# Performance work log

Hardware: AMD Instinct MI355X
Metric: run time of the kernel (lower is better)

The kernel has to match this reference:

```python
import jax, jax.numpy as jnp
import numpy as np

N = 262144   # number of samples (graph edges)
D = 32       # in_features; 'delta_t' is column 0
H = D - 1    # hidden width of each bucket MLP
K = 21       # number of time buckets


def setup_inputs() -> dict:
    key = jax.random.key(0)
    ks = jax.random.split(key, 7)
    x = jax.random.uniform(ks[0], (N, D), dtype=jnp.float32)
    x = x.at[:, 0].set(x[:, 0] * 2.1)  # delta_t in (0, 2.1] -> hits all 21 buckets
    s = 1.0 / np.sqrt(H).astype(np.float32)
    a = jax.random.normal(ks[1], (H,), jnp.float32)           # FeatureTransform scale a_i
    b = jax.random.normal(ks[2], (H,), jnp.float32) * 0.1     # FeatureTransform bias b_i
    W1 = jax.random.normal(ks[3], (K, H, H), jnp.float32) * s # layer_blocks weights
    b1 = jax.random.normal(ks[4], (K, H), jnp.float32) * s
    W2 = jax.random.normal(ks[5], (K, H), jnp.float32) * s    # layer_blocks2 weights (out=1)
    b2 = jax.random.normal(ks[6], (K,), jnp.float32) * s
    return {"x": x, "a": a, "b": b, "W1": W1, "b1": b1, "W2": W2, "b2": b2}


def reference(x, a, b, W1, b1, W2, b2):
    # delta_t column is NOT feature-transformed; all other columns are.
    # Note: the torch code mutates x in place, so x_without_t sees the
    # transformed features while t is the raw delta_t.
    t = x[:, 0]                                   # [N]
    feats = x[:, 1:] * a + b                      # FeatureTransform: a_i*x_i + b_i, [N,H]
    # All 21 bucket branches: Linear -> LeakyReLU(0.1) -> Linear(H,1)
    h = jnp.einsum('nd,kde->kne', feats, W1) + b1[:, None, :]   # [K,N,H]
    h = jnp.where(h >= 0, h, 0.1 * h)                           # LeakyReLU(0.1)
    out = jnp.einsum('kne,ke->kn', h, W2) + b2[:, None]         # [K,N]
    # bucket mask: start < t <= end with edges 0.0,0.1,...,2.0,1000
    edges = jnp.concatenate([jnp.arange(K, dtype=jnp.float32) / 10.0,
                             jnp.array([1000.0], dtype=jnp.float32)])
    valid = (t[None, :] > edges[:-1, None]) & (t[None, :] <= edges[1:, None])  # [K,N]
    return (out * valid.astype(out.dtype)).sum(axis=0)[:, None]  # [N,1]
```

## Files before the change

### kernel.cpp

```cpp
#include <hip/hip_runtime.h>
#include <hip/hip_bf16.h>

#define NN 262144
#define DD 32
#define HH 31
#define KK 21
#define ROWS 256
#define FSTRIDE 18

typedef __attribute__((ext_vector_type(8))) short bf16x8;
typedef __attribute__((ext_vector_type(4))) float f32x4;
typedef __attribute__((ext_vector_type(2))) unsigned int u32x2;
typedef __attribute__((ext_vector_type(4))) unsigned int u32x4;

static __device__ __forceinline__ unsigned short f2bf(float f) {
    __hip_bfloat16 h = __float2bfloat16(f);
    return __builtin_bit_cast(unsigned short, h);
}
static __device__ __forceinline__ unsigned pack2(float lo, float hi) {
    return (unsigned)f2bf(lo) | ((unsigned)f2bf(hi) << 16);
}

__global__ __launch_bounds__(64) void prep_kernel(
    const float* __restrict__ W1, const float* __restrict__ b1,
    const float* __restrict__ W2,
    bf16x8* __restrict__ A0tab, bf16x8* __restrict__ A1tab,
    f32x4* __restrict__ cq0b, f32x4* __restrict__ cq0w,
    f32x4* __restrict__ cq1b, f32x4* __restrict__ cq1w)
{
    const int k = (int)blockIdx.x;
    const int lane = (int)threadIdx.x;
    const int lrow = lane & 15, lgrp = lane >> 4;
    const float* __restrict__ W1k = W1 + k * HH * HH;
    const int e0 = lrow, e1 = 16 + lrow;

    bf16x8 A0, A1;
    #pragma unroll
    for (int j = 0; j < 4; ++j) {
        const int d1 = 4 * lgrp + j;
        const int d2 = 16 + 4 * lgrp + j;
        A0[j]     = (short)f2bf(W1k[d1 * HH + e0]);
        A0[4 + j] = (d2 < HH) ? (short)f2bf(W1k[d2 * HH + e0]) : (short)0;
        A1[j]     = (e1 < HH) ? (short)f2bf(W1k[d1 * HH + e1]) : (short)0;
        A1[4 + j] = (e1 < HH && d2 < HH) ? (short)f2bf(W1k[d2 * HH + e1]) : (short)0;
    }
    A0tab[k * 64 + lane] = A0;
    A1tab[k * 64 + lane] = A1;

    f32x4 b0v, w0v, b1v, w1v;
    #pragma unroll
    for (int r = 0; r < 4; ++r) {
        const int e = 4 * lgrp + r, eb = 16 + e;
        b0v[r] = b1[k * HH + e];
        w0v[r] = W2[k * HH + e];
        b1v[r] = (eb < HH) ? b1[k * HH + eb] : 0.0f;
        w1v[r] = (eb < HH) ? W2[k * HH + eb] : 0.0f;
    }
    cq0b[k * 64 + lane] = b0v;
    cq0w[k * 64 + lane] = w0v;
    cq1b[k * 64 + lane] = b1v;
    cq1w[k * 64 + lane] = w1v;
}

__global__ __launch_bounds__(256, 6) void fused_kernel(
    const float* __restrict__ x,
    const float* __restrict__ a,
    const float* __restrict__ b,
    const float* __restrict__ b2,
    const bf16x8* __restrict__ A0tab, const bf16x8* __restrict__ A1tab,
    const f32x4* __restrict__ cq0b, const f32x4* __restrict__ cq0w,
    const f32x4* __restrict__ cq1b, const f32x4* __restrict__ cq1w,
    float* __restrict__ out)
{
    __shared__ unsigned fbf[ROWS * FSTRIDE];
    __shared__ int cnt[KK];
    __shared__ int rnk[KK];
    __shared__ int sbase[KK];
    __shared__ int tstart[KK + 1];
    __shared__ unsigned short sorted[ROWS];

    const int tid = (int)threadIdx.x;
    const int rowbase = (int)blockIdx.x * ROWS;

    if (tid < KK) { cnt[tid] = 0; rnk[tid] = 0; }
    __syncthreads();

    const float* __restrict__ xr = x + (size_t)(rowbase + tid) * DD;
    float4 c[8];
    #pragma unroll
    for (int i = 0; i < 8; ++i) c[i] = ((const float4*)xr)[i];
    const float t = c[0].x;

    const float edges[KK + 1] = {
        0.0f, 0.1f, 0.2f, 0.3f, 0.4f, 0.5f, 0.6f, 0.7f, 0.8f, 0.9f, 1.0f,
        1.1f, 1.2f, 1.3f, 1.4f, 1.5f, 1.6f, 1.7f, 1.8f, 1.9f, 2.0f, 1000.0f
    };
    int kq = -1;
    #pragma unroll
    for (int j = 0; j < KK; ++j)
        if (t > edges[j] && t <= edges[j + 1]) kq = j;

    unsigned* __restrict__ frow = fbf + tid * FSTRIDE;
    #pragma unroll
    for (int s = 0; s < 8; ++s) {
        const float f0 = fmaf(c[s].y, a[4 * s + 0], b[4 * s + 0]);
        const float f1 = fmaf(c[s].z, a[4 * s + 1], b[4 * s + 1]);
        const float f2 = fmaf(c[s].w, a[4 * s + 2], b[4 * s + 2]);
        const float f3 = (s < 7) ? fmaf(c[s + 1].x, a[4 * s + 3], b[4 * s + 3]) : 0.0f;
        frow[2 * s]     = pack2(f0, f1);
        frow[2 * s + 1] = pack2(f2, f3);
    }

    if (kq >= 0) atomicAdd(&cnt[kq], 1);
    else out[rowbase + tid] = 0.0f;
    __syncthreads();

    if (tid == 0) {
        int s = 0, ts = 0;
        #pragma unroll
        for (int j = 0; j < KK; ++j) {
            sbase[j] = s; tstart[j] = ts;
            s += cnt[j]; ts += (cnt[j] + 15) >> 4;
        }
        tstart[KK] = ts;
    }
    __syncthreads();
    if (kq >= 0) {
        const int r = atomicAdd(&rnk[kq], 1);
        sorted[sbase[kq] + r] = (unsigned short)tid;
    }
    __syncthreads();

    const int lane = tid & 63;
    const int wave = tid >> 6;
    const int lrow = lane & 15;
    const int lgrp = lane >> 4;

    const int NT = tstart[KK];
    const int ts_l = tstart[(lane <= KK) ? lane : KK];

    for (int tix = wave; tix < NT; tix += 4) {
        const unsigned long long m = __ballot(ts_l <= tix);
        const int k = __builtin_amdgcn_readfirstlane(__popcll(m) - 1);

        const int sb = sbase[k];
        const int cn = cnt[k];
        const int r0 = (tix - tstart[k]) * 16;
        const int rl = r0 + lrow;

        const int R = sorted[sb + ((rl < cn) ? rl : 0)];

        const unsigned* __restrict__ fr = fbf + R * FSTRIDE;
        const u32x2 wlo = *(const u32x2*)(fr + 2 * lgrp);
        const u32x2 whi = *(const u32x2*)(fr + 8 + 2 * lgrp);
        u32x4 bw;
        bw[0] = wlo[0]; bw[1] = wlo[1]; bw[2] = whi[0]; bw[3] = whi[1];
        const bf16x8 B = __builtin_bit_cast(bf16x8, bw);

        const bf16x8 A0 = A0tab[k * 64 + lane];
        const bf16x8 A1 = A1tab[k * 64 + lane];
        const f32x4 cb0 = cq0b[k * 64 + lane];
        const f32x4 cw0 = cq0w[k * 64 + lane];
        const f32x4 cb1 = cq1b[k * 64 + lane];
        const f32x4 cw1 = cq1w[k * 64 + lane];
        const float b2k = b2[k];

        f32x4 acc0 = {0.0f, 0.0f, 0.0f, 0.0f};
        f32x4 acc1 = {0.0f, 0.0f, 0.0f, 0.0f};
        acc0 = __builtin_amdgcn_mfma_f32_16x16x32_bf16(A0, B, acc0, 0, 0, 0);
        acc1 = __builtin_amdgcn_mfma_f32_16x16x32_bf16(A1, B, acc1, 0, 0, 0);

        float S = 0.0f;
        #pragma unroll
        for (int r = 0; r < 4; ++r) {
            const float h0 = acc0[r] + cb0[r];
            const float q0 = (h0 >= 0.0f) ? h0 : 0.1f * h0;
            S = fmaf(q0, cw0[r], S);
            const float h1 = acc1[r] + cb1[r];
            const float q1 = (h1 >= 0.0f) ? h1 : 0.1f * h1;
            S = fmaf(q1, cw1[r], S);
        }
        S += __shfl_xor(S, 16);
        S += __shfl_xor(S, 32);

        if (lgrp == 0 && rl < cn) out[rowbase + R] = S + b2k;
    }
}

extern "C" void kernel_launch(void* const* d_in, const int* in_sizes, int n_in,
                              void* d_out, int out_size, void* d_ws, size_t ws_size,
                              hipStream_t stream) {
    const float* x  = (const float*)d_in[0];
    const float* a  = (const float*)d_in[1];
    const float* b  = (const float*)d_in[2];
    const float* W1 = (const float*)d_in[3];
    const float* b1 = (const float*)d_in[4];
    const float* W2 = (const float*)d_in[5];
    const float* b2 = (const float*)d_in[6];
    float* out = (float*)d_out;

    char* ws = (char*)d_ws;
    bf16x8* A0tab = (bf16x8*)ws;
    bf16x8* A1tab = A0tab + KK * 64;
    f32x4* cq0b = (f32x4*)(A1tab + KK * 64);
    f32x4* cq0w = cq0b + KK * 64;
    f32x4* cq1b = cq0w + KK * 64;
    f32x4* cq1w = cq1b + KK * 64;

    hipLaunchKernelGGL(prep_kernel, dim3(KK), dim3(64), 0, stream,
                       W1, b1, W2, A0tab, A1tab, cq0b, cq0w, cq1b, cq1w);

    hipLaunchKernelGGL(fused_kernel, dim3(NN / ROWS), dim3(256), 0, stream,
                       x, a, b, b2, A0tab, A1tab, cq0b, cq0w, cq1b, cq1w, out);
}
```

Baseline: 21.38 us.

## Split each row across two threads, halve rows per block, parallel-scan bucket offsets

Each block now handles 128 rows with 256 threads, so two threads share a row and each loads half of it (four float4s) and transforms sixteen features; the missing boundary element comes from a lane shuffle. The serial single-thread prefix over bucket counts becomes a wave-level shuffle scan, and the occupancy hint rises to 8 blocks per SM. The aim is fewer registers per thread, more latency hiding on the x loads, and a shorter serial section. The cost is twice as many blocks, each with fewer 16-row MFMA tiles, so partially filled bucket tiles make up a larger share of the work.

```diff
diff --git a/kernel.cpp b/kernel.cpp
--- a/kernel.cpp
+++ b/kernel.cpp
@@ -5,7 +5,7 @@
 #define DD 32
 #define HH 31
 #define KK 21
-#define ROWS 256
+#define ROWS 128
 #define FSTRIDE 18
 
 typedef __attribute__((ext_vector_type(8))) short bf16x8;
@@ -62,7 +62,7 @@
     cq1w[k * 64 + lane] = w1v;
 }
 
-__global__ __launch_bounds__(256, 6) void fused_kernel(
+__global__ __launch_bounds__(256, 8) void fused_kernel(
     const float* __restrict__ x,
     const float* __restrict__ a,
     const float* __restrict__ b,
@@ -80,17 +80,23 @@
     __shared__ unsigned short sorted[ROWS];
 
     const int tid = (int)threadIdx.x;
+    const int lane = tid & 63;
     const int rowbase = (int)blockIdx.x * ROWS;
 
     if (tid < KK) { cnt[tid] = 0; rnk[tid] = 0; }
     __syncthreads();
 
-    const float* __restrict__ xr = x + (size_t)(rowbase + tid) * DD;
-    float4 c[8];
-    #pragma unroll
-    for (int i = 0; i < 8; ++i) c[i] = ((const float4*)xr)[i];
+    const int r    = tid >> 1;
+    const int half = tid & 1;
+    const float4* __restrict__ p =
+        reinterpret_cast<const float4*>(x) + (size_t)blockIdx.x * (ROWS * DD / 4) + tid * 4;
+    float4 c[4];
+    #pragma unroll
+    for (int i = 0; i < 4; ++i) c[i] = p[i];
+
+    const float e16 = __shfl(c[0].x, lane + 1);
+
     const float t = c[0].x;
-
     const float edges[KK + 1] = {
         0.0f, 0.1f, 0.2f, 0.3f, 0.4f, 0.5f, 0.6f, 0.7f, 0.8f, 0.9f, 1.0f,
         1.1f, 1.2f, 1.3f, 1.4f, 1.5f, 1.6f, 1.7f, 1.8f, 1.9f, 2.0f, 1000.0f
@@ -100,38 +106,57 @@
     for (int j = 0; j < KK; ++j)
         if (t > edges[j] && t <= edges[j + 1]) kq = j;
 
-    unsigned* __restrict__ frow = fbf + tid * FSTRIDE;
-    #pragma unroll
-    for (int s = 0; s < 8; ++s) {
-        const float f0 = fmaf(c[s].y, a[4 * s + 0], b[4 * s + 0]);
-        const float f1 = fmaf(c[s].z, a[4 * s + 1], b[4 * s + 1]);
-        const float f2 = fmaf(c[s].w, a[4 * s + 2], b[4 * s + 2]);
-        const float f3 = (s < 7) ? fmaf(c[s + 1].x, a[4 * s + 3], b[4 * s + 3]) : 0.0f;
-        frow[2 * s]     = pack2(f0, f1);
-        frow[2 * s + 1] = pack2(f2, f3);
-    }
-
-    if (kq >= 0) atomicAdd(&cnt[kq], 1);
-    else out[rowbase + tid] = 0.0f;
-    __syncthreads();
-
-    if (tid == 0) {
-        int s = 0, ts = 0;
-        #pragma unroll
-        for (int j = 0; j < KK; ++j) {
-            sbase[j] = s; tstart[j] = ts;
-            s += cnt[j]; ts += (cnt[j] + 15) >> 4;
-        }
-        tstart[KK] = ts;
-    }
-    __syncthreads();
-    if (kq >= 0) {
-        const int r = atomicAdd(&rnk[kq], 1);
-        sorted[sbase[kq] + r] = (unsigned short)tid;
-    }
-    __syncthreads();
-
-    const int lane = tid & 63;
+    unsigned* __restrict__ frow = fbf + r * FSTRIDE + half * 8;
+    if (half == 0) {
+        float f[16];
+        #pragma unroll
+        for (int j = 0; j < 15; ++j) {
+            const float xe = (j + 1 < 4)  ? ((j + 1 == 1) ? c[0].y : (j + 1 == 2) ? c[0].z : c[0].w)
+                                          : ((const float*)c)[j + 1];
+            f[j] = fmaf(xe, a[j], b[j]);
+        }
+        f[15] = fmaf(e16, a[15], b[15]);
+        #pragma unroll
+        for (int s = 0; s < 8; ++s) frow[s] = pack2(f[2 * s], f[2 * s + 1]);
+    } else {
+        float f[16];
+        #pragma unroll
+        for (int j = 0; j < 15; ++j) {
+            const float xe = ((const float*)c)[j + 1];
+            f[j] = fmaf(xe, a[16 + j], b[16 + j]);
+        }
+        f[15] = 0.0f;
+        #pragma unroll
+        for (int s = 0; s < 8; ++s) frow[s] = pack2(f[2 * s], f[2 * s + 1]);
+    }
+
+    if (half == 0) {
+        if (kq >= 0) atomicAdd(&cnt[kq], 1);
+        else out[rowbase + r] = 0.0f;
+    }
+    __syncthreads();
+
+    if (tid < 64) {
+        const int j = tid;
+        const int c0 = (j < KK) ? cnt[j] : 0;
+        const int t0 = (j < KK) ? ((c0 + 15) >> 4) : 0;
+        int sc = c0, st = t0;
+        #pragma unroll
+        for (int off = 1; off < 32; off <<= 1) {
+            const int vc = __shfl_up(sc, off);
+            const int vt = __shfl_up(st, off);
+            if (j >= off) { sc += vc; st += vt; }
+        }
+        if (j < KK) { sbase[j] = sc - c0; tstart[j] = st - t0; }
+        if (j == KK) tstart[KK] = st;
+    }
+    __syncthreads();
+    if (half == 0 && kq >= 0) {
+        const int rr = atomicAdd(&rnk[kq], 1);
+        sorted[sbase[kq] + rr] = (unsigned short)r;
+    }
+    __syncthreads();
+
     const int wave = tid >> 6;
     const int lrow = lane & 15;
     const int lgrp = lane >> 4;
@@ -172,13 +197,13 @@
 
         float S = 0.0f;
         #pragma unroll
-        for (int r = 0; r < 4; ++r) {
-            const float h0 = acc0[r] + cb0[r];
+        for (int rr = 0; rr < 4; ++rr) {
+            const float h0 = acc0[rr] + cb0[rr];
             const float q0 = (h0 >= 0.0f) ? h0 : 0.1f * h0;
-            S = fmaf(q0, cw0[r], S);
-            const float h1 = acc1[r] + cb1[r];
+            S = fmaf(q0, cw0[rr], S);
+            const float h1 = acc1[rr] + cb1[rr];
             const float q1 = (h1 >= 0.0f) ? h1 : 0.1f * h1;
-            S = fmaf(q1, cw1[r], S);
+            S = fmaf(q1, cw1[rr], S);
         }
         S += __shfl_xor(S, 16);
         S += __shfl_xor(S, 32);
```

Result: slower. 22.66 us (+6.0%).
